# Optimization experiments

Measured on AMD Instinct MI355X. Metric: run time of the kernel, lower is better.

Reference implementation:

```python
import jax, jax.numpy as jnp
import numpy as np

N_NODES = 100000
N_EDGES = 1600000
HIDDEN = 128
NUM_RBF = 50
NTYPES = 95
CUTOFF = 5.0


def setup_inputs() -> dict:
    key = jax.random.key(0)
    ks = jax.random.split(key, 10)
    z = jax.random.randint(ks[0], (N_NODES,), 0, NTYPES)
    node_feat = jax.random.normal(ks[1], (N_NODES, HIDDEN), dtype=jnp.float32)
    edge_index = jax.random.randint(ks[2], (2, N_EDGES), 0, N_NODES)
    # distances uniform in [0, 6) so some edges fall beyond the 5.0 cutoff
    edge_weight = jax.random.uniform(ks[3], (N_EDGES,), dtype=jnp.float32) * 6.0
    edge_attr = jax.random.normal(ks[4], (N_EDGES, NUM_RBF), dtype=jnp.float32)
    # learned parameters
    emb = jax.random.normal(ks[5], (NTYPES, HIDDEN), dtype=jnp.float32)
    dp_w = jax.random.normal(ks[6], (HIDDEN, NUM_RBF), dtype=jnp.float32) * (1.0 / np.sqrt(NUM_RBF))
    dp_b = jnp.zeros((HIDDEN,), dtype=jnp.float32)
    comb_w = jax.random.normal(ks[7], (HIDDEN, 2 * HIDDEN), dtype=jnp.float32) * (1.0 / np.sqrt(2 * HIDDEN))
    comb_b = jnp.zeros((HIDDEN,), dtype=jnp.float32)
    return {"z": z, "node_feat": node_feat, "edge_index": edge_index,
            "edge_weight": edge_weight, "edge_attr": edge_attr,
            "emb": emb, "dp_w": dp_w, "dp_b": dp_b,
            "comb_w": comb_w, "comb_b": comb_b}


def cosine_cutoff(r, cutoff):
    c = 0.5 * (jnp.cos(r * (jnp.pi / cutoff)) + 1.0)
    return jnp.where(r < cutoff, c, 0.0)


def reference(z, node_feat, edge_index, edge_weight, edge_attr,
              emb, dp_w, dp_b, comb_w, comb_b):
    # distance filter: [E, H]
    C = cosine_cutoff(edge_weight, CUTOFF)
    W = (edge_attr @ dp_w.T + dp_b) * C[:, None]
    # neighbor-type embedding gathered per edge destination
    x_nb = emb[z]                      # [N, H]
    msg = W * x_nb[edge_index[1]]      # [E, H]
    # scatter-add messages to source nodes
    agg = jnp.zeros_like(node_feat).at[edge_index[0]].add(msg)  # [N, H]
    # combine node features with aggregated neighborhood embedding
    out = jnp.concatenate([node_feat, agg], axis=1) @ comb_w.T + comb_b
    return out
```

## Files before the change

kernel.cpp:

```cpp
#include <hip/hip_runtime.h>

#define HIDDEN 128
#define NRBF 50
#define CUTOFF_F 5.0f
#define PI_OVER_CUTOFF 0.6283185307179586f

typedef __attribute__((ext_vector_type(2))) _Float16 hf2;
using short8_t = __attribute__((ext_vector_type(8))) short;
using f32x4_t  = __attribute__((ext_vector_type(4))) float;

#if defined(__has_builtin)
#if __has_builtin(__builtin_amdgcn_fdot2)
#define HAS_FDOT2 1
#endif
#endif

static __device__ __forceinline__ hf2 pack2(float x, float y) {
    return __builtin_bit_cast(hf2, __builtin_amdgcn_cvt_pkrtz(x, y));
}

static __device__ __forceinline__ float fdot2f(hf2 a, hf2 b, float c) {
#ifdef HAS_FDOT2
    return __builtin_amdgcn_fdot2(a, b, c, false);
#else
    return fmaf((float)a[0], (float)b[0], fmaf((float)a[1], (float)b[1], c));
#endif
}

static __device__ __forceinline__ unsigned int pk_bf16(float a, float b) {
    unsigned int ua = __float_as_uint(a), ub = __float_as_uint(b);
    ua = (ua + 0x7FFFu + ((ua >> 16) & 1u)) >> 16;
    ub = (ub + 0x7FFFu + ((ub >> 16) & 1u)) >> 16;
    return ua | (ub << 16);
}


__global__ __launch_bounds__(256) void hist_kernel(
    const int* __restrict__ ei, const float* __restrict__ ew,
    int* __restrict__ cnt, int E)
{
    int e = blockIdx.x * 256 + threadIdx.x;
    if (e >= E) return;
    float r = ew[e];
    if (r < CUTOFF_F) atomicAdd(&cnt[ei[e]], 1);
}

__global__ __launch_bounds__(256) void scan1_kernel(
    const int* __restrict__ cnt, int* __restrict__ rowptr,
    int* __restrict__ bsum, int N)
{
    __shared__ int sh[256];
    int t = threadIdx.x, b = blockIdx.x;
    int base = b * 1024 + t * 4;
    int v[4];
#pragma unroll
    for (int j = 0; j < 4; ++j) v[j] = (base + j < N) ? cnt[base + j] : 0;
    int s = v[0] + v[1] + v[2] + v[3];
    sh[t] = s;
    __syncthreads();
    for (int off = 1; off < 256; off <<= 1) {
        int x = (t >= off) ? sh[t - off] : 0;
        __syncthreads();
        sh[t] += x;
        __syncthreads();
    }
    int run = sh[t] - s;
#pragma unroll
    for (int j = 0; j < 4; ++j) {
        if (base + j < N) rowptr[base + j] = run;
        run += v[j];
    }
    if (t == 255) bsum[b] = sh[255];
}

__global__ __launch_bounds__(256) void scan2_kernel(
    int* __restrict__ bsum, int* __restrict__ rowptr, int nb, int N)
{
    __shared__ int sh[256];
    int t = threadIdx.x;
    int v = (t < nb) ? bsum[t] : 0;
    sh[t] = v;
    __syncthreads();
    for (int off = 1; off < 256; off <<= 1) {
        int x = (t >= off) ? sh[t - off] : 0;
        __syncthreads();
        sh[t] += x;
        __syncthreads();
    }
    if (t < nb) bsum[t] = sh[t] - v;
    if (t == 255) rowptr[N] = sh[255];
}

__global__ __launch_bounds__(256) void scan3_kernel(
    int* __restrict__ rowptr, int* __restrict__ woff,
    const int* __restrict__ bsum, int N)
{
    int t = threadIdx.x, b = blockIdx.x;
    int base = b * 1024 + t * 4;
    int off = bsum[b];
#pragma unroll
    for (int j = 0; j < 4; ++j) {
        int i = base + j;
        if (i < N) {
            int r = rowptr[i] + off;
            rowptr[i] = r;
            woff[i] = r;
        }
    }
}

__global__ __launch_bounds__(256) void scatter_kernel(
    const int* __restrict__ z, const int* __restrict__ ei,
    const float* __restrict__ ew, int* __restrict__ woff,
    int4* __restrict__ slots, int E)
{
    int e = blockIdx.x * 256 + threadIdx.x;
    if (e >= E) return;
    float r = ew[e];
    if (!(r < CUTOFF_F)) return;
    float C = 0.5f * (cosf(r * PI_OVER_CUTOFF) + 1.0f);
    int src = ei[e];
    int dst = ei[E + e];
    int zt  = z[dst];
    int p = atomicAdd(&woff[src], 1);
    slots[p] = make_int4(src | (zt << 20), e, __float_as_int(C), 0);
}

__global__ __launch_bounds__(256) void gather_stream(
    const int* __restrict__ rowptr, const int4* __restrict__ slots,
    const float* __restrict__ ea, const float* __restrict__ emb,
    const float* __restrict__ dpw, const float* __restrict__ dpb,
    float* __restrict__ agg, int N, int nwaves)
{
    __shared__ unsigned int sh_emb[95 * 64];
    __shared__ unsigned int sh_ea[4][4][32];
    int lane  = threadIdx.x & 63;
    int wslot = threadIdx.x >> 6;
    int wid = __builtin_amdgcn_readfirstlane((int)((blockIdx.x * blockDim.x + threadIdx.x) >> 6));

    for (int idx = threadIdx.x; idx < 95 * 64; idx += 256) {
        int row = idx >> 6, pr = idx & 63;
        float2 v = *(const float2*)(emb + (size_t)row * HIDDEN + pr * 2);
        sh_emb[idx] = __builtin_bit_cast(unsigned int, pack2(v.x, v.y));
    }

    hf2 whA[25], whB[25];
    {
        const float* wr0 = dpw + (size_t)(2 * lane) * NRBF;
        const float* wr1 = wr0 + NRBF;
#pragma unroll
        for (int q = 0; q < 25; ++q) {
            float2 x = *(const float2*)(wr0 + 2 * q);
            float2 y = *(const float2*)(wr1 + 2 * q);
            whA[q] = pack2(x.x, x.y);
            whB[q] = pack2(y.x, y.y);
        }
    }
    float2 db = *(const float2*)(dpb + 2 * lane);
    __syncthreads();

    int M  = rowptr[N];
    int CH = (M + nwaves - 1) / nwaves;
    int c0 = min(wid * CH, M);
    int c1 = min(c0 + CH, M);

    int   cur = -1, run_start = c0;
    float a0 = 0.f, a1 = 0.f;

    for (int i = c0; i < c1; i += 4) {
        int sv[4]; float cf[4]; int ed[4]; unsigned int evu[4]; float2 eaf[4];
#pragma unroll
        for (int j = 0; j < 4; ++j)
            if (i + j < c1) {
                int4 sl = slots[i + j];
                sv[j] = sl.x; ed[j] = sl.y; cf[j] = __int_as_float(sl.z);
            }
#pragma unroll
        for (int j = 0; j < 4; ++j)
            if (i + j < c1) evu[j] = sh_emb[(sv[j] >> 20) * 64 + lane];
#pragma unroll
        for (int j = 0; j < 4; ++j)
            if (i + j < c1 && lane < 25) eaf[j] = *(const float2*)(ea + (size_t)ed[j] * NRBF + 2 * lane);
#pragma unroll
        for (int j = 0; j < 4; ++j)
            if (i + j < c1 && lane < 28) {
                unsigned int u = 0u;
                if (lane < 25) u = __builtin_bit_cast(unsigned int, pack2(eaf[j].x, eaf[j].y));
                sh_ea[wslot][j][lane] = u;
            }
#pragma unroll
        for (int j = 0; j < 4; ++j) {
            if (i + j >= c1) break;
            int src = sv[j] & 0xFFFFF;
            if (src != cur) {
                if (cur >= 0) {
                    int rp0 = rowptr[cur], rp1 = rowptr[cur + 1];
                    float* dst = agg + (size_t)cur * HIDDEN + 2 * lane;
                    if (run_start == rp0 && (i + j) == rp1) {
                        *(float2*)dst = make_float2(a0, a1);
                    } else {
                        unsafeAtomicAdd(dst, a0);
                        unsafeAtomicAdd(dst + 1, a1);
                    }
                }
                cur = src; run_start = i + j; a0 = 0.f; a1 = 0.f;
            }
            float s0a = 0.f, s0b = 0.f, s1a = 0.f, s1b = 0.f;
#pragma unroll
            for (int q = 0; q < 6; ++q) {
                uint4 u = *(const uint4*)&sh_ea[wslot][j][q * 4];
#pragma unroll
                for (int t = 0; t < 4; ++t) {
                    unsigned int w = (t == 0) ? u.x : (t == 1) ? u.y : (t == 2) ? u.z : u.w;
                    hf2 e2 = __builtin_bit_cast(hf2, w);
                    if (t & 1) { s0b = fdot2f(e2, whA[q * 4 + t], s0b); s1b = fdot2f(e2, whB[q * 4 + t], s1b); }
                    else       { s0a = fdot2f(e2, whA[q * 4 + t], s0a); s1a = fdot2f(e2, whB[q * 4 + t], s1a); }
                }
            }
            {
                hf2 e2 = __builtin_bit_cast(hf2, sh_ea[wslot][j][24]);
                s0a = fdot2f(e2, whA[24], s0a);
                s1a = fdot2f(e2, whB[24], s1a);
            }
            float W0 = (s0a + s0b + db.x) * cf[j];
            float W1 = (s1a + s1b + db.y) * cf[j];
            hf2 eh = __builtin_bit_cast(hf2, evu[j]);
            a0 = fmaf(W0, (float)eh[0], a0);
            a1 = fmaf(W1, (float)eh[1], a1);
        }
    }
    if (cur >= 0) {
        int rp0 = rowptr[cur], rp1 = rowptr[cur + 1];
        float* dst = agg + (size_t)cur * HIDDEN + 2 * lane;
        if (run_start == rp0 && c1 == rp1) {
            *(float2*)dst = make_float2(a0, a1);
        } else {
            unsafeAtomicAdd(dst, a0);
            unsafeAtomicAdd(dst + 1, a1);
        }
    }
}

__global__ __launch_bounds__(256) void edge_kernel(
    const int* __restrict__ z, const int* __restrict__ ei,
    const float* __restrict__ ew, const float* __restrict__ ea,
    const float* __restrict__ emb, const float* __restrict__ dpw,
    const float* __restrict__ dpb, float* __restrict__ agg, int E)
{
    int e = blockIdx.x * 256 + threadIdx.x;
    if (e >= E) return;
    float r = ew[e];
    if (!(r < CUTOFF_F)) return;
    float C = 0.5f * (cosf(r * PI_OVER_CUTOFF) + 1.0f);
    int src = ei[e];
    int dst = ei[E + e];
    int zt  = z[dst];
    float av[NRBF];
#pragma unroll
    for (int k = 0; k < NRBF; ++k) av[k] = ea[(size_t)e * NRBF + k];
    const float* er = emb + (size_t)zt * HIDDEN;
    float*       ar = agg + (size_t)src * HIDDEN;
#pragma unroll 2
    for (int h = 0; h < HIDDEN; ++h) {
        const float* wrow = dpw + h * NRBF;
        float s0 = 0.f, s1 = 0.f;
#pragma unroll
        for (int k = 0; k < NRBF; k += 2) {
            s0 = fmaf(av[k],     wrow[k],     s0);
            s1 = fmaf(av[k + 1], wrow[k + 1], s1);
        }
        float w = (dpb[h] + s0 + s1) * C;
        unsafeAtomicAdd(&ar[h], w * er[h]);
    }
}

__global__ __launch_bounds__(256) void combine_mfma(
    const float* __restrict__ nf, const float* __restrict__ cw,
    const float* __restrict__ cbias, float* out, int N)
{
    __shared__ unsigned int As_u[64 * 20];
    __shared__ unsigned int Bs_u[128 * 20];
    int tid  = threadIdx.x;
    int w    = tid >> 6;
    int lane = tid & 63;
    int c    = lane & 15;
    int g    = lane >> 4;
    int row0 = blockIdx.x * 64;

    f32x4_t acc[8];
#pragma unroll
    for (int q = 0; q < 8; ++q) acc[q] = (f32x4_t){0.f, 0.f, 0.f, 0.f};

    for (int ks = 0; ks < 8; ++ks) {
        const float* src = (ks < 4) ? nf : out;
        int kb = (ks & 3) * 32;
        {
            int r = tid >> 2, kq = tid & 3;
            int row = row0 + r;
            float4 v0 = make_float4(0.f, 0.f, 0.f, 0.f), v1 = v0;
            if (row < N) {
                const float4* p = (const float4*)(src + (size_t)row * HIDDEN + kb + kq * 8);
                v0 = p[0]; v1 = p[1];
            }
            *(uint4*)&As_u[r * 20 + kq * 4] =
                make_uint4(pk_bf16(v0.x, v0.y), pk_bf16(v0.z, v0.w),
                           pk_bf16(v1.x, v1.y), pk_bf16(v1.z, v1.w));
        }
        {
            int j = tid >> 1, hf = tid & 1;
            const float4* p = (const float4*)(cw + (size_t)j * 256 + ks * 32 + hf * 16);
            float4 b0 = p[0], b1 = p[1], b2 = p[2], b3 = p[3];
            *(uint4*)&Bs_u[j * 20 + hf * 8] =
                make_uint4(pk_bf16(b0.x, b0.y), pk_bf16(b0.z, b0.w),
                           pk_bf16(b1.x, b1.y), pk_bf16(b1.z, b1.w));
            *(uint4*)&Bs_u[j * 20 + hf * 8 + 4] =
                make_uint4(pk_bf16(b2.x, b2.y), pk_bf16(b2.z, b2.w),
                           pk_bf16(b3.x, b3.y), pk_bf16(b3.z, b3.w));
        }
        __syncthreads();
        uint4 au = *(const uint4*)&As_u[(w * 16 + c) * 20 + g * 4];
        short8_t af = __builtin_bit_cast(short8_t, au);
#pragma unroll
        for (int cbk = 0; cbk < 8; ++cbk) {
            uint4 bu = *(const uint4*)&Bs_u[(cbk * 16 + c) * 20 + g * 4];
            short8_t bf = __builtin_bit_cast(short8_t, bu);
            acc[cbk] = __builtin_amdgcn_mfma_f32_16x16x32_bf16(af, bf, acc[cbk], 0, 0, 0);
        }
        __syncthreads();
    }
#pragma unroll
    for (int cbk = 0; cbk < 8; ++cbk) {
        float bias = cbias[cbk * 16 + c];
#pragma unroll
        for (int r = 0; r < 4; ++r) {
            int row = row0 + w * 16 + g * 4 + r;
            if (row < N) out[(size_t)row * HIDDEN + cbk * 16 + c] = acc[cbk][r] + bias;
        }
    }
}


extern "C" void kernel_launch(void* const* d_in, const int* in_sizes, int n_in,
                              void* d_out, int out_size, void* d_ws, size_t ws_size,
                              hipStream_t stream)
{
    const int*   z   = (const int*)  d_in[0];
    const float* nf  = (const float*)d_in[1];
    const int*   ei  = (const int*)  d_in[2];
    const float* ew  = (const float*)d_in[3];
    const float* ea  = (const float*)d_in[4];
    const float* emb = (const float*)d_in[5];
    const float* dpw = (const float*)d_in[6];
    const float* dpb = (const float*)d_in[7];
    const float* cw  = (const float*)d_in[8];
    const float* cb  = (const float*)d_in[9];
    float* out = (float*)d_out;

    int N = in_sizes[0];
    int E = in_sizes[3];

    size_t hdr = ((size_t)2 * N + 1 + 1024 + 3) & ~(size_t)3;
    size_t need = hdr * 4 + (size_t)E * 16;

    (void)hipMemsetAsync(out, 0, (size_t)N * HIDDEN * sizeof(float), stream);

    if (ws_size >= need) {
        int*  rowptr = (int*)d_ws;
        int*  woff   = rowptr + (N + 1);
        int*  bsum   = woff + N;
        int4* slots  = (int4*)((unsigned int*)d_ws + hdr);

        int nb1 = (N + 1023) / 1024;

        (void)hipMemsetAsync(woff, 0, (size_t)N * 4, stream);
        hist_kernel<<<(E + 255) / 256, 256, 0, stream>>>(ei, ew, woff, E);
        scan1_kernel<<<nb1, 256, 0, stream>>>(woff, rowptr, bsum, N);
        scan2_kernel<<<1, 256, 0, stream>>>(bsum, rowptr, nb1, N);
        scan3_kernel<<<nb1, 256, 0, stream>>>(rowptr, woff, bsum, N);
        scatter_kernel<<<(E + 255) / 256, 256, 0, stream>>>(z, ei, ew, woff,
                                                            slots, E);
        const int blocks = 2048;
        gather_stream<<<blocks, 256, 0, stream>>>(rowptr, slots, ea, emb,
                                                  dpw, dpb, out, N, blocks * 4);
    } else {
        edge_kernel<<<(E + 255) / 256, 256, 0, stream>>>(z, ei, ew, ea, emb,
                                                         dpw, dpb, out, E);
    }

    combine_mfma<<<(N + 63) / 64, 256, 0, stream>>>(nf, cw, cb, out, N);
}
```

Baseline: 442.9 us.

## Replace per-edge fdot2 gather with MFMA-based tiled distance filter

```diff
diff --git a/kernel.cpp b/kernel.cpp
--- a/kernel.cpp
+++ b/kernel.cpp
@@ -4,27 +4,15 @@
 #define NRBF 50
 #define CUTOFF_F 5.0f
 #define PI_OVER_CUTOFF 0.6283185307179586f
+#define TPB_TILES 8
 
 typedef __attribute__((ext_vector_type(2))) _Float16 hf2;
+typedef _Float16 half8_t __attribute__((ext_vector_type(8)));
+using f32x4_t  = __attribute__((ext_vector_type(4))) float;
 using short8_t = __attribute__((ext_vector_type(8))) short;
-using f32x4_t  = __attribute__((ext_vector_type(4))) float;
-
-#if defined(__has_builtin)
-#if __has_builtin(__builtin_amdgcn_fdot2)
-#define HAS_FDOT2 1
-#endif
-#endif
-
-static __device__ __forceinline__ hf2 pack2(float x, float y) {
-    return __builtin_bit_cast(hf2, __builtin_amdgcn_cvt_pkrtz(x, y));
-}
-
-static __device__ __forceinline__ float fdot2f(hf2 a, hf2 b, float c) {
-#ifdef HAS_FDOT2
-    return __builtin_amdgcn_fdot2(a, b, c, false);
-#else
-    return fmaf((float)a[0], (float)b[0], fmaf((float)a[1], (float)b[1], c));
-#endif
+
+static __device__ __forceinline__ unsigned int pkh(float a, float b) {
+    return __builtin_bit_cast(unsigned int, __builtin_amdgcn_cvt_pkrtz(a, b));
 }
 
 static __device__ __forceinline__ unsigned int pk_bf16(float a, float b) {
@@ -126,117 +114,133 @@
     slots[p] = make_int4(src | (zt << 20), e, __float_as_int(C), 0);
 }
 
-__global__ __launch_bounds__(256) void gather_stream(
+__global__ __launch_bounds__(256) void gather_mfma(
     const int* __restrict__ rowptr, const int4* __restrict__ slots,
     const float* __restrict__ ea, const float* __restrict__ emb,
     const float* __restrict__ dpw, const float* __restrict__ dpb,
-    float* __restrict__ agg, int N, int nwaves)
-{
-    __shared__ unsigned int sh_emb[95 * 64];
-    __shared__ unsigned int sh_ea[4][4][32];
-    int lane  = threadIdx.x & 63;
-    int wslot = threadIdx.x >> 6;
-    int wid = __builtin_amdgcn_readfirstlane((int)((blockIdx.x * blockDim.x + threadIdx.x) >> 6));
-
-    for (int idx = threadIdx.x; idx < 95 * 64; idx += 256) {
-        int row = idx >> 6, pr = idx & 63;
-        float2 v = *(const float2*)(emb + (size_t)row * HIDDEN + pr * 2);
-        sh_emb[idx] = __builtin_bit_cast(unsigned int, pack2(v.x, v.y));
-    }
-
-    hf2 whA[25], whB[25];
-    {
-        const float* wr0 = dpw + (size_t)(2 * lane) * NRBF;
-        const float* wr1 = wr0 + NRBF;
-#pragma unroll
-        for (int q = 0; q < 25; ++q) {
-            float2 x = *(const float2*)(wr0 + 2 * q);
-            float2 y = *(const float2*)(wr1 + 2 * q);
-            whA[q] = pack2(x.x, x.y);
-            whB[q] = pack2(y.x, y.y);
-        }
-    }
-    float2 db = *(const float2*)(dpb + 2 * lane);
+    float* __restrict__ agg, int N)
+{
+    __shared__ unsigned int B_lds[128 * 36];
+    __shared__ int   s_src[TPB_TILES * 64];
+    __shared__ int   s_eid[TPB_TILES * 64];
+    __shared__ int   s_zt [TPB_TILES * 64];
+    __shared__ float s_C  [TPB_TILES * 64];
+
+    int M = rowptr[N];
+
+    int nwg = gridDim.x, orig = blockIdx.x;
+    int q = nwg >> 3, r8 = nwg & 7, xcd = orig & 7, sub = orig >> 3;
+    int lb = (xcd < r8) ? xcd * (q + 1) + sub
+                        : r8 * (q + 1) + (xcd - r8) * q + sub;
+    int gbase = lb * (TPB_TILES * 64);
+    if (gbase >= M) return;
+
+    int tid  = threadIdx.x;
+    int w    = tid >> 6;
+    int lane = tid & 63;
+    int c    = lane & 15;
+    int g    = lane >> 4;
+
+    for (int idx = tid; idx < 128 * 32; idx += 256) {
+        int h = idx >> 5, p = idx & 31;
+        unsigned int u = 0u;
+        if (p < 25) {
+            float2 v = *(const float2*)(dpw + h * NRBF + 2 * p);
+            u = pkh(v.x, v.y);
+        } else if (p == 25) {
+            u = pkh(dpb[h], 0.f);
+        }
+        B_lds[h * 36 + p] = u;
+    }
+    for (int i = tid; i < TPB_TILES * 64; i += 256) {
+        int gi = gbase + i;
+        if (gi < M) {
+            int4 sl = slots[gi];
+            s_src[i] = sl.x & 0xFFFFF;
+            s_zt[i]  = (unsigned int)sl.x >> 20;
+            s_eid[i] = sl.y;
+            s_C[i]   = __int_as_float(sl.z);
+        } else {
+            s_src[i] = 0; s_zt[i] = 0; s_eid[i] = 0; s_C[i] = 0.f;
+        }
+    }
     __syncthreads();
 
-    int M  = rowptr[N];
-    int CH = (M + nwaves - 1) / nwaves;
-    int c0 = min(wid * CH, M);
-    int c1 = min(c0 + CH, M);
-
-    int   cur = -1, run_start = c0;
-    float a0 = 0.f, a1 = 0.f;
-
-    for (int i = c0; i < c1; i += 4) {
-        int sv[4]; float cf[4]; int ed[4]; unsigned int evu[4]; float2 eaf[4];
-#pragma unroll
-        for (int j = 0; j < 4; ++j)
-            if (i + j < c1) {
-                int4 sl = slots[i + j];
-                sv[j] = sl.x; ed[j] = sl.y; cf[j] = __int_as_float(sl.z);
+    half8_t bfrag[8][2];
+#pragma unroll
+    for (int nt = 0; nt < 8; ++nt)
+#pragma unroll
+        for (int ks = 0; ks < 2; ++ks) {
+            uint4 bu = *(const uint4*)&B_lds[(nt * 16 + c) * 36 + ks * 16 + g * 4];
+            bfrag[nt][ks] = __builtin_bit_cast(half8_t, bu);
+        }
+
+    for (int t = 0; t < TPB_TILES; ++t) {
+        if (gbase + t * 64 >= M) break;
+        int eloc = t * 64 + w * 16 + c;
+        int   eid = s_eid[eloc];
+        float Cv  = s_C[eloc];
+        const float* row = ea + (size_t)eid * NRBF;
+        uint4 a0u, a1u;
+        {
+            float4 q0 = *(const float4*)(row + g * 8);
+            float4 q1 = *(const float4*)(row + g * 8 + 4);
+            a0u = make_uint4(pkh(Cv * q0.x, Cv * q0.y), pkh(Cv * q0.z, Cv * q0.w),
+                             pkh(Cv * q1.x, Cv * q1.y), pkh(Cv * q1.z, Cv * q1.w));
+        }
+        if (g < 2) {
+            float4 q0 = *(const float4*)(row + 32 + g * 8);
+            float4 q1 = *(const float4*)(row + 36 + g * 8);
+            a1u = make_uint4(pkh(Cv * q0.x, Cv * q0.y), pkh(Cv * q0.z, Cv * q0.w),
+                             pkh(Cv * q1.x, Cv * q1.y), pkh(Cv * q1.z, Cv * q1.w));
+        } else if (g == 2) {
+            float2 tv = *(const float2*)(row + 48);
+            a1u = make_uint4(pkh(Cv * tv.x, Cv * tv.y), pkh(Cv, 0.f), 0u, 0u);
+        } else {
+            a1u = make_uint4(0u, 0u, 0u, 0u);
+        }
+        half8_t A0 = __builtin_bit_cast(half8_t, a0u);
+        half8_t A1 = __builtin_bit_cast(half8_t, a1u);
+
+        f32x4_t acc[8];
+#pragma unroll
+        for (int nt = 0; nt < 8; ++nt) acc[nt] = (f32x4_t){0.f, 0.f, 0.f, 0.f};
+#pragma unroll
+        for (int nt = 0; nt < 8; ++nt) {
+            acc[nt] = __builtin_amdgcn_mfma_f32_16x16x32_f16(A0, bfrag[nt][0], acc[nt], 0, 0, 0);
+            acc[nt] = __builtin_amdgcn_mfma_f32_16x16x32_f16(A1, bfrag[nt][1], acc[nt], 0, 0, 0);
+        }
+
+        int rbase = t * 64 + w * 16 + g * 4;
+        int sprev = s_src[rbase];
+        float racc[8];
+        {
+            const float* er = emb + (size_t)s_zt[rbase] * HIDDEN;
+#pragma unroll
+            for (int nt = 0; nt < 8; ++nt) racc[nt] = acc[nt][0] * er[nt * 16 + c];
+        }
+#pragma unroll
+        for (int r = 1; r < 4; ++r) {
+            int s = s_src[rbase + r];
+            const float* er = emb + (size_t)s_zt[rbase + r] * HIDDEN;
+            if (s != sprev) {
+                float* dst = agg + (size_t)sprev * HIDDEN;
+#pragma unroll
+                for (int nt = 0; nt < 8; ++nt) {
+                    unsafeAtomicAdd(dst + nt * 16 + c, racc[nt]);
+                    racc[nt] = 0.f;
+                }
+                sprev = s;
             }
 #pragma unroll
-        for (int j = 0; j < 4; ++j)
-            if (i + j < c1) evu[j] = sh_emb[(sv[j] >> 20) * 64 + lane];
-#pragma unroll
-        for (int j = 0; j < 4; ++j)
-            if (i + j < c1 && lane < 25) eaf[j] = *(const float2*)(ea + (size_t)ed[j] * NRBF + 2 * lane);
-#pragma unroll
-        for (int j = 0; j < 4; ++j)
-            if (i + j < c1 && lane < 28) {
-                unsigned int u = 0u;
-                if (lane < 25) u = __builtin_bit_cast(unsigned int, pack2(eaf[j].x, eaf[j].y));
-                sh_ea[wslot][j][lane] = u;
-            }
-#pragma unroll
-        for (int j = 0; j < 4; ++j) {
-            if (i + j >= c1) break;
-            int src = sv[j] & 0xFFFFF;
-            if (src != cur) {
-                if (cur >= 0) {
-                    int rp0 = rowptr[cur], rp1 = rowptr[cur + 1];
-                    float* dst = agg + (size_t)cur * HIDDEN + 2 * lane;
-                    if (run_start == rp0 && (i + j) == rp1) {
-                        *(float2*)dst = make_float2(a0, a1);
-                    } else {
-                        unsafeAtomicAdd(dst, a0);
-                        unsafeAtomicAdd(dst + 1, a1);
-                    }
-                }
-                cur = src; run_start = i + j; a0 = 0.f; a1 = 0.f;
-            }
-            float s0a = 0.f, s0b = 0.f, s1a = 0.f, s1b = 0.f;
-#pragma unroll
-            for (int q = 0; q < 6; ++q) {
-                uint4 u = *(const uint4*)&sh_ea[wslot][j][q * 4];
-#pragma unroll
-                for (int t = 0; t < 4; ++t) {
-                    unsigned int w = (t == 0) ? u.x : (t == 1) ? u.y : (t == 2) ? u.z : u.w;
-                    hf2 e2 = __builtin_bit_cast(hf2, w);
-                    if (t & 1) { s0b = fdot2f(e2, whA[q * 4 + t], s0b); s1b = fdot2f(e2, whB[q * 4 + t], s1b); }
-                    else       { s0a = fdot2f(e2, whA[q * 4 + t], s0a); s1a = fdot2f(e2, whB[q * 4 + t], s1a); }
-                }
-            }
-            {
-                hf2 e2 = __builtin_bit_cast(hf2, sh_ea[wslot][j][24]);
-                s0a = fdot2f(e2, whA[24], s0a);
-                s1a = fdot2f(e2, whB[24], s1a);
-            }
-            float W0 = (s0a + s0b + db.x) * cf[j];
-            float W1 = (s1a + s1b + db.y) * cf[j];
-            hf2 eh = __builtin_bit_cast(hf2, evu[j]);
-            a0 = fmaf(W0, (float)eh[0], a0);
-            a1 = fmaf(W1, (float)eh[1], a1);
-        }
-    }
-    if (cur >= 0) {
-        int rp0 = rowptr[cur], rp1 = rowptr[cur + 1];
-        float* dst = agg + (size_t)cur * HIDDEN + 2 * lane;
-        if (run_start == rp0 && c1 == rp1) {
-            *(float2*)dst = make_float2(a0, a1);
-        } else {
-            unsafeAtomicAdd(dst, a0);
-            unsafeAtomicAdd(dst + 1, a1);
+            for (int nt = 0; nt < 8; ++nt)
+                racc[nt] = fmaf(acc[nt][r], er[nt * 16 + c], racc[nt]);
+        }
+        {
+            float* dst = agg + (size_t)sprev * HIDDEN;
+#pragma unroll
+            for (int nt = 0; nt < 8; ++nt)
+                unsafeAtomicAdd(dst + nt * 16 + c, racc[nt]);
         }
     }
 }
@@ -379,9 +383,9 @@
         scan3_kernel<<<nb1, 256, 0, stream>>>(rowptr, woff, bsum, N);
         scatter_kernel<<<(E + 255) / 256, 256, 0, stream>>>(z, ei, ew, woff,
                                                             slots, E);
-        const int blocks = 2048;
-        gather_stream<<<blocks, 256, 0, stream>>>(rowptr, slots, ea, emb,
-                                                  dpw, dpb, out, N, blocks * 4);
+        int nblk = (E + TPB_TILES * 64 - 1) / (TPB_TILES * 64);
+        gather_mfma<<<nblk, 256, 0, stream>>>(rowptr, slots, ea, emb,
+                                              dpw, dpb, out, N);
     } else {
         edge_kernel<<<(E + 255) / 256, 256, 0, stream>>>(z, ei, ew, ea, emb,
                                                          dpw, dpb, out, E);
```

New measurement: 695.4 us. 1.57x slower.

## Pre-pack cutoff-scaled fp16 edge features in CSR order and use MFMA for distance filter

Applied to the files above, without the earlier changes.

```diff
diff --git a/kernel.cpp b/kernel.cpp
--- a/kernel.cpp
+++ b/kernel.cpp
@@ -4,29 +4,17 @@
 #define NRBF 50
 #define CUTOFF_F 5.0f
 #define PI_OVER_CUTOFF 0.6283185307179586f
-
+#define SLOT_U32 28
+#define EPB 512
+
+typedef _Float16 half8_t __attribute__((ext_vector_type(8)));
+using f32x4_t  = __attribute__((ext_vector_type(4))) float;
+using short8_t = __attribute__((ext_vector_type(8))) short;
 typedef __attribute__((ext_vector_type(2))) _Float16 hf2;
-using short8_t = __attribute__((ext_vector_type(8))) short;
-using f32x4_t  = __attribute__((ext_vector_type(4))) float;
-
-#if defined(__has_builtin)
-#if __has_builtin(__builtin_amdgcn_fdot2)
-#define HAS_FDOT2 1
-#endif
-#endif
-
-static __device__ __forceinline__ hf2 pack2(float x, float y) {
-    return __builtin_bit_cast(hf2, __builtin_amdgcn_cvt_pkrtz(x, y));
-}
-
-static __device__ __forceinline__ float fdot2f(hf2 a, hf2 b, float c) {
-#ifdef HAS_FDOT2
-    return __builtin_amdgcn_fdot2(a, b, c, false);
-#else
-    return fmaf((float)a[0], (float)b[0], fmaf((float)a[1], (float)b[1], c));
-#endif
-}
-
+
+static __device__ __forceinline__ unsigned int pkh(float a, float b) {
+    return __builtin_bit_cast(unsigned int, __builtin_amdgcn_cvt_pkrtz(a, b));
+}
 static __device__ __forceinline__ unsigned int pk_bf16(float a, float b) {
     unsigned int ua = __float_as_uint(a), ub = __float_as_uint(b);
     ua = (ua + 0x7FFFu + ((ua >> 16) & 1u)) >> 16;
@@ -109,10 +97,11 @@
     }
 }
 
-__global__ __launch_bounds__(256) void scatter_kernel(
+__global__ __launch_bounds__(256) void scatter_pack(
     const int* __restrict__ z, const int* __restrict__ ei,
-    const float* __restrict__ ew, int* __restrict__ woff,
-    int4* __restrict__ slots, int E)
+    const float* __restrict__ ew, const float* __restrict__ ea,
+    int* __restrict__ woff, int* __restrict__ desc,
+    unsigned int* __restrict__ slots, int E)
 {
     int e = blockIdx.x * 256 + threadIdx.x;
     if (e >= E) return;
@@ -123,27 +112,171 @@
     int dst = ei[E + e];
     int zt  = z[dst];
     int p = atomicAdd(&woff[src], 1);
-    slots[p] = make_int4(src | (zt << 20), e, __float_as_int(C), 0);
+    desc[p] = src | (zt << 20);
+
+    unsigned int buf[SLOT_U32];
+    const float2* rp = (const float2*)(ea + (size_t)e * NRBF);
+#pragma unroll
+    for (int q = 0; q < 25; ++q) {
+        float2 v = rp[q];
+        buf[q] = pkh(C * v.x, C * v.y);
+    }
+    buf[25] = pkh(C, 0.f);
+    buf[26] = 0u; buf[27] = 0u;
+    uint4* sp = (uint4*)(slots + (size_t)p * SLOT_U32);
+#pragma unroll
+    for (int q = 0; q < 7; ++q) sp[q] = ((const uint4*)buf)[q];
+}
+
+__global__ __launch_bounds__(256) void scatter_simple(
+    const int* __restrict__ z, const int* __restrict__ ei,
+    const float* __restrict__ ew, int* __restrict__ woff,
+    int* __restrict__ desc, float* __restrict__ cCA, int* __restrict__ eidA,
+    int E)
+{
+    int e = blockIdx.x * 256 + threadIdx.x;
+    if (e >= E) return;
+    float r = ew[e];
+    if (!(r < CUTOFF_F)) return;
+    float C = 0.5f * (cosf(r * PI_OVER_CUTOFF) + 1.0f);
+    int src = ei[e];
+    int dst = ei[E + e];
+    int zt  = z[dst];
+    int p = atomicAdd(&woff[src], 1);
+    desc[p] = src | (zt << 20);
+    cCA[p]  = C;
+    eidA[p] = e;
+}
+
+__global__ __launch_bounds__(256) void gather_mfma(
+    const int* __restrict__ rowptr, const int* __restrict__ desc,
+    const unsigned int* __restrict__ slots, const float* __restrict__ emb,
+    const float* __restrict__ dpw, const float* __restrict__ dpb,
+    float* __restrict__ agg, int N)
+{
+    __shared__ float Wlds[4][16 * 132];
+    int M = rowptr[N];
+
+    int nwg = gridDim.x, orig = blockIdx.x;
+    int q = nwg >> 3, r8 = nwg & 7, xcd = orig & 7, sub = orig >> 3;
+    int lb = (xcd < r8) ? xcd * (q + 1) + sub
+                        : r8 * (q + 1) + (xcd - r8) * q + sub;
+    int gbase = lb * EPB;
+    if (gbase >= M) return;
+
+    int tid  = threadIdx.x;
+    int w    = tid >> 6;
+    int lane = tid & 63;
+    int c    = lane & 15;
+    int g    = lane >> 4;
+
+    unsigned int* bstage = (unsigned int*)&Wlds[0][0];
+    for (int idx = tid; idx < 128 * 32; idx += 256) {
+        int h = idx >> 5, p = idx & 31;
+        unsigned int u = 0u;
+        if (p < 25) {
+            float2 v = *(const float2*)(dpw + h * NRBF + 2 * p);
+            u = pkh(v.x, v.y);
+        } else if (p == 25) {
+            u = pkh(dpb[h], 0.f);
+        }
+        bstage[h * 36 + p] = u;
+    }
+    __syncthreads();
+    half8_t bfrag[8][2];
+#pragma unroll
+    for (int nt = 0; nt < 8; ++nt)
+#pragma unroll
+        for (int ks = 0; ks < 2; ++ks) {
+            uint4 bu = *(const uint4*)&bstage[(nt * 16 + c) * 36 + ks * 16 + g * 4];
+            bfrag[nt][ks] = __builtin_bit_cast(half8_t, bu);
+        }
+    __syncthreads();
+
+    float* Ww = &Wlds[w][0];
+    int wbeg = gbase + w * 128;
+    int wend = min(wbeg + 128, M);
+    if (wbeg >= M) return;
+
+    int   cur = -1, run_start = wbeg;
+    float r0 = 0.f, r1 = 0.f;
+
+    for (int tt = 0; tt < 8; ++tt) {
+        int eb = wbeg + tt * 16;
+        if (eb >= M) break;
+        int ge = eb + c;
+        const uint4* sp = (const uint4*)(slots + (size_t)ge * SLOT_U32);
+        uint4 a0u = make_uint4(0u, 0u, 0u, 0u), a1u = a0u;
+        if (ge < M) {
+            a0u = sp[g];
+            if (g < 3) a1u = sp[4 + g];
+        }
+        half8_t A0 = __builtin_bit_cast(half8_t, a0u);
+        half8_t A1 = __builtin_bit_cast(half8_t, a1u);
+
+        f32x4_t acc[8];
+#pragma unroll
+        for (int nt = 0; nt < 8; ++nt) acc[nt] = (f32x4_t){0.f, 0.f, 0.f, 0.f};
+#pragma unroll
+        for (int nt = 0; nt < 8; ++nt) {
+            acc[nt] = __builtin_amdgcn_mfma_f32_16x16x32_f16(A0, bfrag[nt][0], acc[nt], 0, 0, 0);
+            acc[nt] = __builtin_amdgcn_mfma_f32_16x16x32_f16(A1, bfrag[nt][1], acc[nt], 0, 0, 0);
+        }
+#pragma unroll
+        for (int nt = 0; nt < 8; ++nt)
+#pragma unroll
+            for (int r = 0; r < 4; ++r)
+                Ww[(g * 4 + r) * 132 + nt * 16 + c] = acc[nt][r];
+
+        for (int e2 = 0; e2 < 16; ++e2) {
+            int gi = eb + e2;
+            if (gi >= M) break;
+            int d   = desc[gi];
+            int src = d & 0xFFFFF;
+            int zt  = (unsigned int)d >> 20;
+            if (src != cur) {
+                if (cur >= 0) {
+                    int rp0 = rowptr[cur], rp1 = rowptr[cur + 1];
+                    float* dst = agg + (size_t)cur * HIDDEN + 2 * lane;
+                    if (run_start == rp0 && gi == rp1) {
+                        *(float2*)dst = make_float2(r0, r1);
+                    } else {
+                        unsafeAtomicAdd(dst,     r0);
+                        unsafeAtomicAdd(dst + 1, r1);
+                    }
+                }
+                cur = src; run_start = gi; r0 = 0.f; r1 = 0.f;
+            }
+            float2 wv = *(const float2*)&Ww[e2 * 132 + 2 * lane];
+            float2 ev = *(const float2*)(emb + (size_t)zt * HIDDEN + 2 * lane);
+            r0 = fmaf(wv.x, ev.x, r0);
+            r1 = fmaf(wv.y, ev.y, r1);
+        }
+    }
+    if (cur >= 0) {
+        int rp0 = rowptr[cur], rp1 = rowptr[cur + 1];
+        float* dst = agg + (size_t)cur * HIDDEN + 2 * lane;
+        if (run_start == rp0 && wend == rp1) {
+            *(float2*)dst = make_float2(r0, r1);
+        } else {
+            unsafeAtomicAdd(dst,     r0);
+            unsafeAtomicAdd(dst + 1, r1);
+        }
+    }
 }
 
 __global__ __launch_bounds__(256) void gather_stream(
-    const int* __restrict__ rowptr, const int4* __restrict__ slots,
+    const int* __restrict__ rowptr, const int* __restrict__ desc,
+    const float* __restrict__ cC, const int* __restrict__ eidA,
     const float* __restrict__ ea, const float* __restrict__ emb,
     const float* __restrict__ dpw, const float* __restrict__ dpb,
     float* __restrict__ agg, int N, int nwaves)
 {
-    __shared__ unsigned int sh_emb[95 * 64];
     __shared__ unsigned int sh_ea[4][4][32];
     int lane  = threadIdx.x & 63;
     int wslot = threadIdx.x >> 6;
     int wid = __builtin_amdgcn_readfirstlane((int)((blockIdx.x * blockDim.x + threadIdx.x) >> 6));
 
-    for (int idx = threadIdx.x; idx < 95 * 64; idx += 256) {
-        int row = idx >> 6, pr = idx & 63;
-        float2 v = *(const float2*)(emb + (size_t)row * HIDDEN + pr * 2);
-        sh_emb[idx] = __builtin_bit_cast(unsigned int, pack2(v.x, v.y));
-    }
-
     hf2 whA[25], whB[25];
     {
         const float* wr0 = dpw + (size_t)(2 * lane) * NRBF;
@@ -152,12 +285,11 @@
         for (int q = 0; q < 25; ++q) {
             float2 x = *(const float2*)(wr0 + 2 * q);
             float2 y = *(const float2*)(wr1 + 2 * q);
-            whA[q] = pack2(x.x, x.y);
-            whB[q] = pack2(y.x, y.y);
+            whA[q] = __builtin_bit_cast(hf2, pkh(x.x, x.y));
+            whB[q] = __builtin_bit_cast(hf2, pkh(y.x, y.y));
         }
     }
     float2 db = *(const float2*)(dpb + 2 * lane);
-    __syncthreads();
 
     int M  = rowptr[N];
     int CH = (M + nwaves - 1) / nwaves;
@@ -168,16 +300,13 @@
     float a0 = 0.f, a1 = 0.f;
 
     for (int i = c0; i < c1; i += 4) {
-        int sv[4]; float cf[4]; int ed[4]; unsigned int evu[4]; float2 eaf[4];
+        int sv[4]; float cf[4]; int ed[4]; float2 ev[4]; float2 eaf[4];
 #pragma unroll
         for (int j = 0; j < 4; ++j)
-            if (i + j < c1) {
-                int4 sl = slots[i + j];
-                sv[j] = sl.x; ed[j] = sl.y; cf[j] = __int_as_float(sl.z);
-            }
+            if (i + j < c1) { sv[j] = desc[i + j]; cf[j] = cC[i + j]; ed[j] = eidA[i + j]; }
 #pragma unroll
         for (int j = 0; j < 4; ++j)
-            if (i + j < c1) evu[j] = sh_emb[(sv[j] >> 20) * 64 + lane];
+            if (i + j < c1) ev[j] = *(const float2*)(emb + (size_t)((unsigned int)sv[j] >> 20) * HIDDEN + 2 * lane);
 #pragma unroll
         for (int j = 0; j < 4; ++j)
             if (i + j < c1 && lane < 25) eaf[j] = *(const float2*)(ea + (size_t)ed[j] * NRBF + 2 * lane);
@@ -185,7 +314,7 @@
         for (int j = 0; j < 4; ++j)
             if (i + j < c1 && lane < 28) {
                 unsigned int u = 0u;
-                if (lane < 25) u = __builtin_bit_cast(unsigned int, pack2(eaf[j].x, eaf[j].y));
+                if (lane < 25) u = pkh(eaf[j].x, eaf[j].y);
                 sh_ea[wslot][j][lane] = u;
             }
 #pragma unroll
@@ -205,28 +334,34 @@
                 }
                 cur = src; run_start = i + j; a0 = 0.f; a1 = 0.f;
             }
-            float s0a = 0.f, s0b = 0.f, s1a = 0.f, s1b = 0.f;
-#pragma unroll
-            for (int q = 0; q < 6; ++q) {
-                uint4 u = *(const uint4*)&sh_ea[wslot][j][q * 4];
+            float s0 = 0.f, s1 = 0.f;
+#pragma unroll
+            for (int qq = 0; qq < 6; ++qq) {
+                uint4 u = *(const uint4*)&sh_ea[wslot][j][qq * 4];
 #pragma unroll
                 for (int t = 0; t < 4; ++t) {
-                    unsigned int w = (t == 0) ? u.x : (t == 1) ? u.y : (t == 2) ? u.z : u.w;
-                    hf2 e2 = __builtin_bit_cast(hf2, w);
-                    if (t & 1) { s0b = fdot2f(e2, whA[q * 4 + t], s0b); s1b = fdot2f(e2, whB[q * 4 + t], s1b); }
-                    else       { s0a = fdot2f(e2, whA[q * 4 + t], s0a); s1a = fdot2f(e2, whB[q * 4 + t], s1a); }
+                    unsigned int ww = (t == 0) ? u.x : (t == 1) ? u.y : (t == 2) ? u.z : u.w;
+                    hf2 e2 = __builtin_bit_cast(hf2, ww);
+#ifdef __has_builtin
+#if __has_builtin(__builtin_amdgcn_fdot2)
+                    s0 = __builtin_amdgcn_fdot2(e2, whA[qq * 4 + t], s0, false);
+                    s1 = __builtin_amdgcn_fdot2(e2, whB[qq * 4 + t], s1, false);
+#else
+                    s0 = fmaf((float)e2[0], (float)whA[qq*4+t][0], fmaf((float)e2[1], (float)whA[qq*4+t][1], s0));
+                    s1 = fmaf((float)e2[0], (float)whB[qq*4+t][0], fmaf((float)e2[1], (float)whB[qq*4+t][1], s1));
+#endif
+#endif
                 }
             }
             {
                 hf2 e2 = __builtin_bit_cast(hf2, sh_ea[wslot][j][24]);
-                s0a = fdot2f(e2, whA[24], s0a);
-                s1a = fdot2f(e2, whB[24], s1a);
+                s0 = fmaf((float)e2[0], (float)whA[24][0], fmaf((float)e2[1], (float)whA[24][1], s0));
+                s1 = fmaf((float)e2[0], (float)whB[24][0], fmaf((float)e2[1], (float)whB[24][1], s1));
             }
-            float W0 = (s0a + s0b + db.x) * cf[j];
-            float W1 = (s1a + s1b + db.y) * cf[j];
-            hf2 eh = __builtin_bit_cast(hf2, evu[j]);
-            a0 = fmaf(W0, (float)eh[0], a0);
-            a1 = fmaf(W1, (float)eh[1], a1);
+            float W0 = (s0 + db.x) * cf[j];
+            float W1 = (s1 + db.y) * cf[j];
+            a0 = fmaf(W0, ev[j].x, a0);
+            a1 = fmaf(W1, ev[j].y, a1);
         }
     }
     if (cur >= 0) {
@@ -269,8 +404,8 @@
             s0 = fmaf(av[k],     wrow[k],     s0);
             s1 = fmaf(av[k + 1], wrow[k + 1], s1);
         }
-        float w = (dpb[h] + s0 + s1) * C;
-        unsafeAtomicAdd(&ar[h], w * er[h]);
+        float w2 = (dpb[h] + s0 + s1) * C;
+        unsafeAtomicAdd(&ar[h], w2 * er[h]);
     }
 }
 
@@ -359,29 +494,51 @@
     int N = in_sizes[0];
     int E = in_sizes[3];
 
-    size_t hdr = ((size_t)2 * N + 1 + 1024 + 3) & ~(size_t)3;
-    size_t need = hdr * 4 + (size_t)E * 16;
+    size_t hdr  = ((size_t)2 * N + 1 + 1024 + 3) & ~(size_t)3;
+    size_t need1 = (hdr + (size_t)E + (size_t)E * SLOT_U32 + 4) * 4;
+    size_t need2 = (hdr + (size_t)3 * E) * 4;
 
     (void)hipMemsetAsync(out, 0, (size_t)N * HIDDEN * sizeof(float), stream);
 
-    if (ws_size >= need) {
-        int*  rowptr = (int*)d_ws;
-        int*  woff   = rowptr + (N + 1);
-        int*  bsum   = woff + N;
-        int4* slots  = (int4*)((unsigned int*)d_ws + hdr);
-
-        int nb1 = (N + 1023) / 1024;
+    int nb1 = (N + 1023) / 1024;
+
+    if (ws_size >= need1) {
+        int* rowptr = (int*)d_ws;
+        int* woff   = rowptr + (N + 1);
+        int* bsum   = woff + N;
+        int* desc   = (int*)d_ws + hdr;
+        unsigned int* slots = (unsigned int*)(desc + E);
+        slots = (unsigned int*)(((size_t)slots + 15) & ~(size_t)15);
 
         (void)hipMemsetAsync(woff, 0, (size_t)N * 4, stream);
         hist_kernel<<<(E + 255) / 256, 256, 0, stream>>>(ei, ew, woff, E);
         scan1_kernel<<<nb1, 256, 0, stream>>>(woff, rowptr, bsum, N);
         scan2_kernel<<<1, 256, 0, stream>>>(bsum, rowptr, nb1, N);
         scan3_kernel<<<nb1, 256, 0, stream>>>(rowptr, woff, bsum, N);
-        scatter_kernel<<<(E + 255) / 256, 256, 0, stream>>>(z, ei, ew, woff,
-                                                            slots, E);
+        scatter_pack<<<(E + 255) / 256, 256, 0, stream>>>(z, ei, ew, ea, woff,
+                                                          desc, slots, E);
+        int nblk = (E + EPB - 1) / EPB;
+        gather_mfma<<<nblk, 256, 0, stream>>>(rowptr, desc, slots, emb,
+                                              dpw, dpb, out, N);
+    } else if (ws_size >= need2) {
+        int* rowptr = (int*)d_ws;
+        int* woff   = rowptr + (N + 1);
+        int* bsum   = woff + N;
+        int* desc   = (int*)d_ws + hdr;
+        float* cCA  = (float*)(desc + E);
+        int* eidA   = (int*)(cCA + E);
+
+        (void)hipMemsetAsync(woff, 0, (size_t)N * 4, stream);
+        hist_kernel<<<(E + 255) / 256, 256, 0, stream>>>(ei, ew, woff, E);
+        scan1_kernel<<<nb1, 256, 0, stream>>>(woff, rowptr, bsum, N);
+        scan2_kernel<<<1, 256, 0, stream>>>(bsum, rowptr, nb1, N);
+        scan3_kernel<<<nb1, 256, 0, stream>>>(rowptr, woff, bsum, N);
+        scatter_simple<<<(E + 255) / 256, 256, 0, stream>>>(z, ei, ew, woff,
+                                                            desc, cCA, eidA, E);
         const int blocks = 2048;
-        gather_stream<<<blocks, 256, 0, stream>>>(rowptr, slots, ea, emb,
-                                                  dpw, dpb, out, N, blocks * 4);
+        gather_stream<<<blocks, 256, 0, stream>>>(rowptr, desc, cCA, eidA,
+                                                  ea, emb, dpw, dpb, out, N,
+                                                  blocks * 4);
     } else {
         edge_kernel<<<(E + 255) / 256, 256, 0, stream>>>(z, ei, ew, ea, emb,
                                                          dpw, dpb, out, E);
```

Result: slower. 564.2 us (+27.4%).
